# Performance work log

Hardware: AMD Instinct MI355X
Metric: run time of the kernel (lower is better)

## Reference

```python
import jax, jax.numpy as jnp
import numpy as np

N_OBJ = 256   # number of RoIs/objects
C = 151       # num_obj_classes (Visual Genome)
H = 512       # hidden_dim == output_dim
T = 3         # time_step


def setup_inputs() -> dict:
    key = jax.random.key(0)
    ks = jax.random.split(key, 12)
    s = jnp.float32(0.02)

    def lin(k, out_dim, in_dim):
        k1, k2 = jax.random.split(k)
        w = jax.random.normal(k1, (out_dim, in_dim), jnp.float32) * s
        b = jax.random.normal(k2, (out_dim,), jnp.float32) * s
        return w, b

    inp = {}
    inp['input_ggnn'] = jax.random.normal(ks[0], (N_OBJ, H), jnp.float32)
    inp['matrix'] = jax.random.uniform(ks[1], (C, C), jnp.float32)
    for i, name in enumerate(['eq3_w', 'eq3_u', 'eq4_w', 'eq4_u', 'eq5_w', 'eq5_u']):
        in_dim = 2 * H if name.endswith('_w') else H
        w, b = lin(ks[2 + i], H, in_dim)
        inp['w_' + name] = w
        inp['b_' + name] = b
    w, b = lin(ks[8], H, 2 * H)
    inp['w_out'], inp['b_out'] = w, b
    w, b = lin(ks[9], C, C * H)
    inp['w_cls'], inp['b_cls'] = w, b
    return inp


def _ggnn_obj(input_ggnn, matrix,
              w_eq3_w, b_eq3_w, w_eq3_u, b_eq3_u,
              w_eq4_w, b_eq4_w, w_eq4_u, b_eq4_u,
              w_eq5_w, b_eq5_w, w_eq5_u, b_eq5_u,
              w_out, b_out, w_cls, b_cls):
    n = input_ggnn.shape[0]
    # hidden[i, c] = input_ggnn[i] for every class slot c  -> [N, C, H]
    hidden0 = jnp.broadcast_to(input_ggnn[:, None, :], (n, C, H))

    def step(hidden, _):
        hidden_sum = hidden.sum(axis=0)                # [C, H]
        x = hidden_sum[None, :, :] - hidden            # [N, C, H]
        # matrix.T @ x_i  and  matrix @ x_i, vectorized over N
        av1 = jnp.einsum('cd,nch->ndh', matrix, x)     # M^T propagation
        av2 = jnp.einsum('dc,nch->ndh', matrix, x)     # M propagation
        av = jnp.concatenate([av1, av2], axis=-1).reshape(n * C, 2 * H)
        h = hidden.reshape(n * C, H)
        zv = jax.nn.sigmoid(av @ w_eq3_w.T + b_eq3_w + h @ w_eq3_u.T + b_eq3_u)
        rv = jax.nn.sigmoid(av @ w_eq4_w.T + b_eq4_w + h @ w_eq4_u.T + b_eq4_u)
        hv = jnp.tanh(av @ w_eq5_w.T + b_eq5_w + (rv * h) @ w_eq5_u.T + b_eq5_u)
        h = (1.0 - zv) * h + zv * hv
        return h.reshape(n, C, H), None

    hidden, _ = jax.lax.scan(step, hidden0, None, length=T)

    inp_rep = hidden0.reshape(n * C, H)                # input repeated per class slot
    out = jnp.concatenate([hidden.reshape(n * C, H), inp_rep], axis=1)  # [N*C, 2H]
    out = jax.nn.relu(out @ w_out.T + b_out)           # [N*C, H]
    obj_dists = out.reshape(n, C * H) @ w_cls.T + b_cls  # [N, C]
    return obj_dists


def reference(input_ggnn, matrix,
              w_eq3_w, b_eq3_w, w_eq3_u, b_eq3_u,
              w_eq4_w, b_eq4_w, w_eq4_u, b_eq4_u,
              w_eq5_w, b_eq5_w, w_eq5_u, b_eq5_u,
              w_out, b_out, w_cls, b_cls):
    return _ggnn_obj(input_ggnn, matrix,
                     w_eq3_w, b_eq3_w, w_eq3_u, b_eq3_u,
                     w_eq4_w, b_eq4_w, w_eq4_u, b_eq4_u,
                     w_eq5_w, b_eq5_w, w_eq5_u, b_eq5_u,
                     w_out, b_out, w_cls, b_cls)
```

## Files before the change

kernel.cpp:

```cpp
#include <hip/hip_runtime.h>


#define C_     151
#define H_     512
#define NOBJ   256
#define NR     38656
#define NCH    64
#define CH     9664
#define CHP    9728
#define KPAD   160
#define KLDS   168
#define KA     2560
#define KV     3584

typedef _Float16 half8 __attribute__((ext_vector_type(8)));
typedef _Float16 half4 __attribute__((ext_vector_type(4)));
typedef float    f32x4 __attribute__((ext_vector_type(4)));

__device__ __forceinline__ float sigm(float x) { return 1.f / (1.f + expf(-x)); }

__device__ __forceinline__ void gload16(const void* g, void* l) {
    __builtin_amdgcn_global_load_lds(
        (const __attribute__((address_space(1))) void*)g,
        (__attribute__((address_space(3))) void*)l, 16, 0, 0);
}

__device__ __forceinline__ half8 loadA8(const _Float16* p) { return *(const half8*)p; }
__device__ __forceinline__ half8 loadA8(const float* p) {
    f32x4 a = *(const f32x4*)p;
    f32x4 b = *(const f32x4*)(p + 4);
    half8 o;
    #pragma unroll
    for (int j = 0; j < 4; ++j) { o[j] = (_Float16)a[j]; o[4 + j] = (_Float16)b[j]; }
    return o;
}

template<int OP, typename AT, bool DUPK>
__global__ __launch_bounds__(256, 2)
void gemm_kernel(const AT* __restrict__ A, int lda,
                 const _Float16* __restrict__ B, int ldb,
                 void* __restrict__ Out, int ldo,
                 const float* __restrict__ bias,
                 const float* __restrict__ bias2,
                 int kchunk, int chunkStride)
{
    constexpr bool A16 = (sizeof(AT) == 2);
    __shared__ _Float16 sA[128 * 32];
    __shared__ _Float16 sB[128 * 32];
    const int tid  = threadIdx.x;
    const int lane = tid & 63;
    const int w    = tid >> 6;
    const int m0   = blockIdx.x * 128;
    const int n0   = blockIdx.y * 128;
    const int kbase = blockIdx.z * kchunk;

    const int s0 = tid, s1 = tid + 256;
    const AT* Ap0 = A + (size_t)(m0 + (s0 >> 2)) * lda + 8 * (s0 & 3);
    const AT* Ap1 = A + (size_t)(m0 + (s1 >> 2)) * lda + 8 * (s1 & 3);
    const _Float16* Bp0 = B + (size_t)(n0 + (s0 >> 2)) * ldb + kbase + 8 * (s0 & 3);
    const _Float16* Bp1 = B + (size_t)(n0 + (s1 >> 2)) * ldb + kbase + 8 * (s1 & 3);
    const int la0 = 8 * s0;
    const int la1 = 8 * s1;
    _Float16* lA0 = &sA[w * 512];
    _Float16* lA1 = &sA[2048 + w * 512];
    _Float16* lB0 = &sB[w * 512];
    _Float16* lB1 = &sB[2048 + w * 512];

    f32x4 acc[4][4];
    #pragma unroll
    for (int i = 0; i < 4; ++i)
        #pragma unroll
        for (int j = 0; j < 4; ++j)
            #pragma unroll
            for (int r = 0; r < 4; ++r) acc[i][j][r] = 0.f;

    const int mrow = (w >> 1) * 64;
    const int ncol = (w & 1) * 64;
    const int fra  = (lane & 15) * 32 + 8 * (lane >> 4);

    for (int k0 = 0; k0 < kchunk; k0 += 32) {
        int kA;
        if (DUPK) kA = (k0 < 2048) ? k0 : ((k0 < 3072) ? k0 - 2048 : k0 - 1024);
        else      kA = kbase + k0;
        if constexpr (A16) {
            __syncthreads();
            gload16(Ap0 + kA, lA0);
            gload16(Ap1 + kA, lA1);
            gload16(Bp0 + k0, lB0);
            gload16(Bp1 + k0, lB1);
            __syncthreads();
        } else {
            half8 va0 = loadA8(Ap0 + kA);
            half8 va1 = loadA8(Ap1 + kA);
            half8 vb0 = *(const half8*)(Bp0 + k0);
            half8 vb1 = *(const half8*)(Bp1 + k0);
            __syncthreads();
            *(half8*)&sA[la0] = va0;
            *(half8*)&sA[la1] = va1;
            *(half8*)&sB[la0] = vb0;
            *(half8*)&sB[la1] = vb1;
            __syncthreads();
        }
        half8 af[4], bf[4];
        #pragma unroll
        for (int i = 0; i < 4; ++i)
            af[i] = *(const half8*)&sA[(mrow + i * 16) * 32 + fra];
        #pragma unroll
        for (int i = 0; i < 4; ++i)
            bf[i] = *(const half8*)&sB[(ncol + i * 16) * 32 + fra];
        #pragma unroll
        for (int mi = 0; mi < 4; ++mi)
            #pragma unroll
            for (int ni = 0; ni < 4; ++ni)
                acc[mi][ni] = __builtin_amdgcn_mfma_f32_16x16x32_f16(af[mi], bf[ni], acc[mi][ni], 0, 0, 0);
    }

    const size_t zoff = (size_t)blockIdx.z * (size_t)chunkStride;
    #pragma unroll
    for (int mi = 0; mi < 4; ++mi) {
        #pragma unroll
        for (int ni = 0; ni < 4; ++ni) {
            #pragma unroll
            for (int r = 0; r < 4; ++r) {
                const int row = m0 + mrow + mi * 16 + (lane >> 4) * 4 + r;
                const int col = n0 + ncol + ni * 16 + (lane & 15);
                float v = acc[mi][ni][r];
                const size_t o = zoff + (size_t)row * ldo + col;
                if (OP == 0) {
                    ((float*)Out)[o] = v;
                } else if (OP == 1) {
                    ((_Float16*)Out)[o] = (_Float16)v;
                } else {
                    const unsigned n = (unsigned)row / 151u;
                    v += bias[col] + bias2[n * 512u + col];
                    v = v > 0.f ? v : 0.f;
                    ((_Float16*)Out)[o] = (_Float16)v;
                }
            }
        }
    }
}

template<int OP, bool DUPK>
__global__ __launch_bounds__(512, 2)
void gemm_wide(const _Float16* __restrict__ A, int lda,
               const _Float16* __restrict__ B, int ldb,
               void* __restrict__ Out, int ldo,
               int kchunk, int chunkStride)
{
    __shared__ _Float16 sA[128 * 32];
    __shared__ _Float16 sB[256 * 32];
    const int tid  = threadIdx.x;
    const int lane = tid & 63;
    const int w    = tid >> 6;
    const int m0   = blockIdx.x * 128;
    const int n0   = blockIdx.y * 256;
    const int kbase = blockIdx.z * kchunk;

    const _Float16* Ap = A + (size_t)(m0 + (tid >> 2)) * lda + 8 * (tid & 3);
    const _Float16* Bp0 = B + (size_t)(n0 + (tid >> 2)) * ldb + kbase + 8 * (tid & 3);
    const _Float16* Bp1 = B + (size_t)(n0 + 128 + (tid >> 2)) * ldb + kbase + 8 * (tid & 3);
    _Float16* lA  = &sA[w * 512];
    _Float16* lB0 = &sB[w * 512];
    _Float16* lB1 = &sB[4096 + w * 512];

    f32x4 acc[4][4];
    #pragma unroll
    for (int i = 0; i < 4; ++i)
        #pragma unroll
        for (int j = 0; j < 4; ++j)
            #pragma unroll
            for (int r = 0; r < 4; ++r) acc[i][j][r] = 0.f;

    const int mrow = (w >> 2) * 64;
    const int ncol = (w & 3) * 64;
    const int fra  = (lane & 15) * 32 + 8 * (lane >> 4);

    for (int k0 = 0; k0 < kchunk; k0 += 32) {
        int kA;
        if (DUPK) kA = (k0 < 2048) ? k0 : ((k0 < 3072) ? k0 - 2048 : k0 - 1024);
        else      kA = kbase + k0;
        __syncthreads();
        gload16(Ap + kA, lA);
        gload16(Bp0 + k0, lB0);
        gload16(Bp1 + k0, lB1);
        __syncthreads();
        half8 af[4], bf[4];
        #pragma unroll
        for (int i = 0; i < 4; ++i)
            af[i] = *(const half8*)&sA[(mrow + i * 16) * 32 + fra];
        #pragma unroll
        for (int i = 0; i < 4; ++i)
            bf[i] = *(const half8*)&sB[(ncol + i * 16) * 32 + fra];
        #pragma unroll
        for (int mi = 0; mi < 4; ++mi)
            #pragma unroll
            for (int ni = 0; ni < 4; ++ni)
                acc[mi][ni] = __builtin_amdgcn_mfma_f32_16x16x32_f16(af[mi], bf[ni], acc[mi][ni], 0, 0, 0);
    }

    const size_t zoff = (size_t)blockIdx.z * (size_t)chunkStride;
    #pragma unroll
    for (int mi = 0; mi < 4; ++mi) {
        #pragma unroll
        for (int ni = 0; ni < 4; ++ni) {
            #pragma unroll
            for (int r = 0; r < 4; ++r) {
                const int row = m0 + mrow + mi * 16 + (lane >> 4) * 4 + r;
                const int col = n0 + ncol + ni * 16 + (lane & 15);
                const float v = acc[mi][ni][r];
                const size_t o = zoff + (size_t)row * ldo + col;
                if (OP == 0) ((float*)Out)[o] = v;
                else         ((_Float16*)Out)[o] = (_Float16)v;
            }
        }
    }
}

__global__ __launch_bounds__(256, 2)
void mix_kernel(const _Float16* __restrict__ xh, const _Float16* __restrict__ xl,
                const _Float16* __restrict__ MTh, const _Float16* __restrict__ MTl,
                const _Float16* __restrict__ Mrh, const _Float16* __restrict__ Mrl,
                _Float16* __restrict__ AVH)
{
    __shared__ _Float16 sxh[64 * KLDS];
    __shared__ _Float16 sxl[64 * KLDS];
    const int n  = blockIdx.x;
    const int h0 = blockIdx.y * 64;
    const int tid = threadIdx.x;

    #pragma unroll
    for (int i = 0; i < 5; ++i) {
        const int s  = tid + 256 * i;
        const int c  = s >> 3;
        const int hg = s & 7;
        half8 vh = *(const half8*)&xh[(size_t)(n * C_ + c) * H_ + h0 + hg * 8];
        half8 vl = *(const half8*)&xl[(size_t)(n * C_ + c) * H_ + h0 + hg * 8];
        #pragma unroll
        for (int j = 0; j < 8; ++j) {
            sxh[(hg * 8 + j) * KLDS + c] = vh[j];
            sxl[(hg * 8 + j) * KLDS + c] = vl[j];
        }
    }
    __syncthreads();

    const int lane = tid & 63;
    const int w    = tid >> 6;
    const _Float16* Mhi = (w >> 1) ? Mrh : MTh;
    const _Float16* Mlo = (w >> 1) ? Mrl : MTl;
    const int hb = (w & 1) * 32;

    f32x4 acc[10][2];
    #pragma unroll
    for (int i = 0; i < 10; ++i)
        #pragma unroll
        for (int j = 0; j < 2; ++j)
            #pragma unroll
            for (int r = 0; r < 4; ++r) acc[i][j][r] = 0.f;

    #pragma unroll
    for (int pass = 0; pass < 3; ++pass) {
        const _Float16* Ma = (pass == 2) ? Mlo : Mhi;
        const _Float16* X  = (pass == 1) ? sxl : sxh;
        #pragma unroll
        for (int kk = 0; kk < 5; ++kk) {
            const int k0 = kk * 32;
            half8 bf[2];
            #pragma unroll
            for (int ht = 0; ht < 2; ++ht)
                bf[ht] = *(const half8*)&X[(hb + ht * 16 + (lane & 15)) * KLDS + k0 + 8 * (lane >> 4)];
            #pragma unroll
            for (int dt = 0; dt < 10; ++dt) {
                half8 af = *(const half8*)&Ma[(dt * 16 + (lane & 15)) * KPAD + k0 + 8 * (lane >> 4)];
                acc[dt][0] = __builtin_amdgcn_mfma_f32_16x16x32_f16(af, bf[0], acc[dt][0], 0, 0, 0);
                acc[dt][1] = __builtin_amdgcn_mfma_f32_16x16x32_f16(af, bf[1], acc[dt][1], 0, 0, 0);
            }
        }
    }

    const int mixoff = (w >> 1) * 512;
    #pragma unroll
    for (int dt = 0; dt < 10; ++dt) {
        #pragma unroll
        for (int ht = 0; ht < 2; ++ht) {
            #pragma unroll
            for (int r = 0; r < 4; ++r) {
                const int d = dt * 16 + (lane >> 4) * 4 + r;
                if (d < C_) {
                    const int h = h0 + hb + ht * 16 + (lane & 15);
                    const float v = acc[dt][ht][r];
                    const _Float16 hi = (_Float16)v;
                    const _Float16 lo = (_Float16)(v - (float)hi);
                    _Float16* rowp = AVH + (size_t)(n * C_ + d) * KA + mixoff + h;
                    rowp[0]    = hi;
                    rowp[1024] = lo;
                }
            }
        }
    }
}


__global__ void k_sreduce(const float* __restrict__ hid, float* __restrict__ Stmp)
{
    const int c  = blockIdx.x;
    const int g  = blockIdx.y;
    const int hw = threadIdx.x;
    const float* p = hid + (size_t)c * H_ + hw * 8;
    float s[8];
    #pragma unroll
    for (int j = 0; j < 8; ++j) s[j] = 0.f;
    const size_t stride = (size_t)C_ * H_;
    for (int n = g * 32; n < g * 32 + 32; ++n) {
        f32x4 a = *(const f32x4*)(p + (size_t)n * stride);
        f32x4 b = *(const f32x4*)(p + (size_t)n * stride + 4);
        #pragma unroll
        for (int j = 0; j < 4; ++j) { s[j] += a[j]; s[4 + j] += b[j]; }
    }
    float* o = Stmp + (size_t)g * (C_ * H_) + c * H_ + hw * 8;
    *(f32x4*)o       = f32x4{s[0], s[1], s[2], s[3]};
    *(f32x4*)(o + 4) = f32x4{s[4], s[5], s[6], s[7]};
}

__global__ void k_sfold(const float* __restrict__ Stmp, float* __restrict__ S)
{
    const int idx = blockIdx.x * 256 + threadIdx.x;
    float s = 0.f;
    #pragma unroll
    for (int g = 0; g < 8; ++g) s += Stmp[(size_t)g * (C_ * H_) + idx];
    S[idx] = s;
}

__global__ void k_xcast(const float* __restrict__ hid, const float* __restrict__ S,
                        _Float16* __restrict__ xh, _Float16* __restrict__ xl,
                        _Float16* __restrict__ AVH, int cbase)
{
    const int idx = blockIdx.x * 256 + threadIdx.x;
    const unsigned r = idx >> 6;
    const int h = (idx & 63) * 8;
    half8 oh, ol, hh;
    if (r < CH) {
        const unsigned c = r % 151u;
        const float* hp = &hid[(size_t)(cbase + r) * H_ + h];
        const float* sp = &S[c * H_ + h];
        #pragma unroll
        for (int j = 0; j < 8; ++j) {
            const float hv = hp[j];
            const float x = sp[j] - hv;
            const _Float16 hi = (_Float16)x;
            oh[j] = hi;
            ol[j] = (_Float16)(x - (float)hi);
            hh[j] = (_Float16)hv;
        }
    } else {
        #pragma unroll
        for (int j = 0; j < 8; ++j) { oh[j] = (_Float16)0.f; ol[j] = (_Float16)0.f; hh[j] = (_Float16)0.f; }
    }
    *(half8*)&xh[(size_t)r * H_ + h] = oh;
    *(half8*)&xl[(size_t)r * H_ + h] = ol;
    *(half8*)&AVH[(size_t)r * KA + 2048 + h] = hh;
}

__global__ void k_ew1(_Float16* __restrict__ pre, const float* __restrict__ hid,
                      const float* __restrict__ bz, const float* __restrict__ br, int cbase)
{
    const int idx = blockIdx.x * 256 + threadIdx.x;
    const unsigned r = idx >> 7;
    const int o4 = (idx & 127) << 2;
    const size_t base = (size_t)r * 1536;
    half4 zp = *(const half4*)&pre[base + o4];
    half4 rp = *(const half4*)&pre[base + 512 + o4];
    f32x4 hd = *(const f32x4*)&hid[(size_t)(cbase + r) * H_ + o4];
    f32x4 bz4 = *(const f32x4*)&bz[o4];
    f32x4 br4 = *(const f32x4*)&br[o4];
    half4 zs, rh;
    #pragma unroll
    for (int j = 0; j < 4; ++j) {
        float z = sigm((float)zp[j] + bz4[j]);
        float rr = sigm((float)rp[j] + br4[j]);
        zs[j] = (_Float16)z;
        rh[j] = (_Float16)(rr * hd[j]);
    }
    *(half4*)&pre[base + o4] = zs;
    *(half4*)&pre[base + 512 + o4] = rh;
}

__global__ void k_ew2(const _Float16* __restrict__ pre, const _Float16* __restrict__ p5u,
                      float* __restrict__ hid, const float* __restrict__ b5, int cbase)
{
    const int idx = blockIdx.x * 256 + threadIdx.x;
    const unsigned r = idx >> 7;
    const int o4 = (idx & 127) << 2;
    const size_t base = (size_t)r * 1536;
    half4 w5 = *(const half4*)&pre[base + 1024 + o4];
    half4 p5 = *(const half4*)&p5u[(size_t)r * H_ + o4];
    half4 zz = *(const half4*)&pre[base + o4];
    f32x4 hd = *(const f32x4*)&hid[(size_t)(cbase + r) * H_ + o4];
    f32x4 b54 = *(const f32x4*)&b5[o4];
    #pragma unroll
    for (int j = 0; j < 4; ++j) {
        float t = tanhf((float)w5[j] + (float)p5[j] + b54[j]);
        float z = (float)zz[j];
        hd[j] = (1.f - z) * hd[j] + z * t;
    }
    *(f32x4*)&hid[(size_t)(cbase + r) * H_ + o4] = hd;
}


__global__ void prep_wbig(const float* w3w, const float* w3u,
                          const float* w4w, const float* w4u,
                          const float* w5w, const float* w5u,
                          _Float16* __restrict__ Wbig)
{
    const int idx = blockIdx.x * 256 + threadIdx.x;
    const int op = idx / KV;
    const int j = idx - op * KV;
    const int g = op >> 9, o = op & 511;
    const float* ww = (g == 0) ? w3w : (g == 1) ? w4w : w5w;
    const float* wu = (g == 0) ? w3u : (g == 1) ? w4u : w5u;
    _Float16 out;
    if (j < 1024) {
        out = (_Float16)ww[o * 1024 + j];
    } else if (j < 2048) {
        out = (_Float16)ww[o * 1024 + (j - 1024)];
    } else if (j < 3072) {
        const float v = ww[o * 1024 + (j - 2048)];
        const _Float16 hi = (_Float16)v;
        out = (_Float16)(v - (float)hi);
    } else {
        out = (g < 2) ? (_Float16)wu[o * 512 + (j - 3072)] : (_Float16)0.f;
    }
    Wbig[idx] = out;
}

__global__ void prep_m(const float* __restrict__ matrix,
                       _Float16* __restrict__ MTh, _Float16* __restrict__ MTl,
                       _Float16* __restrict__ Mrh, _Float16* __restrict__ Mrl)
{
    const int idx = blockIdx.x * 256 + threadIdx.x;
    const int d = idx / KPAD, c = idx - d * KPAD;
    float vT = 0.f, vR = 0.f;
    if (d < C_ && c < C_) { vT = matrix[c * C_ + d]; vR = matrix[d * C_ + c]; }
    const _Float16 th = (_Float16)vT;
    const _Float16 rh = (_Float16)vR;
    MTh[idx] = th; MTl[idx] = (_Float16)(vT - (float)th);
    Mrh[idx] = rh; Mrl[idx] = (_Float16)(vR - (float)rh);
}

__global__ void prep_wout(const float* __restrict__ wout,
                          _Float16* __restrict__ WL, _Float16* __restrict__ WR)
{
    const int idx = blockIdx.x * 256 + threadIdx.x;
    const int o = idx >> 9, j = idx & 511;
    WL[idx] = (_Float16)wout[o * 1024 + j];
    WR[idx] = (_Float16)wout[o * 1024 + 512 + j];
}

__global__ void prep_wcls(const float* __restrict__ wcls, _Float16* __restrict__ w16)
{
    const int k = blockIdx.x * 256 + threadIdx.x;
    const int d = blockIdx.y;
    _Float16 v = (_Float16)0.f;
    if (d < C_) v = (_Float16)wcls[(size_t)d * (C_ * H_) + k];
    w16[(size_t)d * (C_ * H_) + k] = v;
}

__global__ void k_cast(const float* __restrict__ src, _Float16* __restrict__ dst, int n)
{
    const int i = blockIdx.x * 256 + threadIdx.x;
    if (i < n) dst[i] = (_Float16)src[i];
}

__global__ void prep_bias(const float* b3w, const float* b3u, const float* b4w,
                          const float* b4u, const float* b5w, const float* b5u,
                          float* bz, float* br, float* b5)
{
    const int i = threadIdx.x;
    bz[i] = b3w[i] + b3u[i];
    br[i] = b4w[i] + b4u[i];
    b5[i] = b5w[i] + b5u[i];
}

__global__ void prep_hid(const float* __restrict__ input, float* __restrict__ hid)
{
    const int idx = blockIdx.x * 256 + threadIdx.x;
    const unsigned row = idx >> 7;
    const int h4 = (idx & 127) << 2;
    const unsigned n = row / 151u;
    f32x4 v = *(const f32x4*)&input[(size_t)n * H_ + h4];
    *(f32x4*)&hid[(size_t)row * H_ + h4] = v;
}

__global__ void k_reduce(const float* __restrict__ partial, const float* __restrict__ bcls,
                         float* __restrict__ out)
{
    const int idx = blockIdx.x * 256 + threadIdx.x;
    const unsigned n = (unsigned)idx / 151u;
    const unsigned d = (unsigned)idx - n * 151u;
    float s = 0.f;
    for (int z = 0; z < C_; ++z)
        s += partial[(size_t)z * (NOBJ * 256) + n * 256 + d];
    out[idx] = s + bcls[d];
}


extern "C" void kernel_launch(void* const* d_in, const int* in_sizes, int n_in,
                              void* d_out, int out_size, void* d_ws, size_t ws_size,
                              hipStream_t stream)
{
    const float* input  = (const float*)d_in[0];
    const float* matrix = (const float*)d_in[1];
    const float* w3w = (const float*)d_in[2];
    const float* b3w = (const float*)d_in[3];
    const float* w3u = (const float*)d_in[4];
    const float* b3u = (const float*)d_in[5];
    const float* w4w = (const float*)d_in[6];
    const float* b4w = (const float*)d_in[7];
    const float* w4u = (const float*)d_in[8];
    const float* b4u = (const float*)d_in[9];
    const float* w5w = (const float*)d_in[10];
    const float* b5w = (const float*)d_in[11];
    const float* w5u = (const float*)d_in[12];
    const float* b5u = (const float*)d_in[13];
    const float* wout = (const float*)d_in[14];
    const float* bout = (const float*)d_in[15];
    const float* wcls = (const float*)d_in[16];
    const float* bcls = (const float*)d_in[17];
    float* obj = (float*)d_out;

    char* ws = (char*)d_ws;
    size_t off = 0;
    auto take = [&](size_t bytes) -> char* {
        off = (off + 255) & ~(size_t)255;
        char* p = ws + off;
        off += bytes;
        return p;
    };

    _Float16* Wbig  = (_Float16*)take((size_t)1536 * KV * 2);
    _Float16* MTh   = (_Float16*)take((size_t)KPAD * KPAD * 2);
    _Float16* MTl   = (_Float16*)take((size_t)KPAD * KPAD * 2);
    _Float16* Mrh   = (_Float16*)take((size_t)KPAD * KPAD * 2);
    _Float16* Mrl   = (_Float16*)take((size_t)KPAD * KPAD * 2);
    _Float16* W5u16 = (_Float16*)take((size_t)512 * 512 * 2);
    _Float16* WL16  = (_Float16*)take((size_t)512 * 512 * 2);
    _Float16* WR16  = (_Float16*)take((size_t)512 * 512 * 2);
    _Float16* in16  = (_Float16*)take((size_t)256 * 512 * 2);
    float*    bz    = (float*)take(512 * 4);
    float*    br    = (float*)take(512 * 4);
    float*    b5    = (float*)take(512 * 4);
    float*    Stmp  = (float*)take((size_t)8 * C_ * H_ * 4);
    float*    S32   = (float*)take((size_t)C_ * H_ * 4);
    float*    base  = (float*)take((size_t)256 * 512 * 4);
    float*    hid32 = (float*)take((size_t)NR * H_ * 4);
    _Float16* AVH   = (_Float16*)take((size_t)CHP * KA * 2);
    _Float16* prec  = (_Float16*)take((size_t)CHP * 1536 * 2);
    _Float16* xh = prec;
    _Float16* xl = prec + (size_t)CHP * H_;
    _Float16* p5u = AVH;
    _Float16* OUT16 = AVH;
    _Float16* Wcls16 = (_Float16*)hid32;
    float* partial = (float*)((char*)hid32 + (size_t)NOBJ * C_ * H_ * 2);

    (void)in_sizes; (void)n_in; (void)out_size; (void)ws_size;

    prep_wbig<<<dim3((1536 * KV) / 256), 256, 0, stream>>>(w3w, w3u, w4w, w4u, w5w, w5u, Wbig);
    prep_m<<<dim3((KPAD * KPAD) / 256), 256, 0, stream>>>(matrix, MTh, MTl, Mrh, Mrl);
    k_cast<<<dim3((512 * 512) / 256), 256, 0, stream>>>(w5u, W5u16, 512 * 512);
    prep_wout<<<dim3((512 * 512) / 256), 256, 0, stream>>>(wout, WL16, WR16);
    k_cast<<<dim3((256 * 512) / 256), 256, 0, stream>>>(input, in16, 256 * 512);
    prep_bias<<<dim3(1), 512, 0, stream>>>(b3w, b3u, b4w, b4u, b5w, b5u, bz, br, b5);
    prep_hid<<<dim3((NR * 128) / 256), 256, 0, stream>>>(input, hid32);
    gemm_kernel<0, _Float16, false><<<dim3(2, 4, 1), 256, 0, stream>>>(
        in16, 512, WR16, 512, base, 512, nullptr, nullptr, 512, 0);

    for (int t = 0; t < 3; ++t) {
        k_sreduce<<<dim3(C_, 8), 64, 0, stream>>>(hid32, Stmp);
        k_sfold<<<dim3((C_ * H_) / 256), 256, 0, stream>>>(Stmp, S32);
        for (int cc = 0; cc < 4; ++cc) {
            const int cbase = cc * CH;
            k_xcast<<<dim3((CHP * 64) / 256), 256, 0, stream>>>(hid32, S32, xh, xl, AVH, cbase);
            mix_kernel<<<dim3(NCH, 8), 256, 0, stream>>>(xh, xl, MTh, MTl, Mrh, Mrl, AVH);
            gemm_wide<1, true><<<dim3(CHP / 128, 1536 / 256, 1), 512, 0, stream>>>(
                AVH, KA, Wbig, KV, prec, 1536, KV, 0);
            k_ew1<<<dim3((CH * 128) / 256), 256, 0, stream>>>(prec, hid32, bz, br, cbase);
            gemm_wide<1, false><<<dim3(CHP / 128, 512 / 256, 1), 512, 0, stream>>>(
                prec + 512, 1536, W5u16, 512, p5u, 512, 512, 0);
            k_ew2<<<dim3((CH * 128) / 256), 256, 0, stream>>>(prec, p5u, hid32, b5, cbase);
        }
    }

    gemm_kernel<2, float, false><<<dim3(NR / 128, 512 / 128, 1), 256, 0, stream>>>(
        hid32, 512, WL16, 512, OUT16, 512, bout, base, 512, 0);

    prep_wcls<<<dim3((C_ * H_) / 256, 256), 256, 0, stream>>>(wcls, Wcls16);
    gemm_kernel<0, _Float16, false><<<dim3(NOBJ / 128, 256 / 128, C_), 256, 0, stream>>>(
        OUT16, C_ * H_, Wcls16, C_ * H_, partial, 256, nullptr, nullptr, 512, NOBJ * 256);
    k_reduce<<<dim3(NR / 256), 256, 0, stream>>>(partial, bcls, obj);
}
```

Baseline: 2.971 ms.

## Swizzle GEMM LDS layout, fuse xcast into mix kernel, split-K the W5u GEMM

Applies an XOR-style swizzle to the K-quarter placement of global-to-LDS loads and fragment reads in both GEMM kernels, aiming to reduce LDS bank conflicts. Folds the k_xcast conversion (S minus hidden, hi/lo fp16 split, hidden cast into AVH) directly into mix_kernel, which removes one launch and the xh/xl round trip through global memory. Replaces the wide W5u GEMM with a 2-way split-K gemm_kernel launch that writes two partial outputs, and k_ew2 now sums both. Split-K adds an extra partial-buffer read, and mix_kernel now does more scattered fp32 loads.

Measured after the change: 2.777 ms. 1.07x faster.

```diff
diff --git a/kernel.cpp b/kernel.cpp
--- a/kernel.cpp
+++ b/kernel.cpp
@@ -25,6 +25,14 @@
         (__attribute__((address_space(3))) void*)l, 16, 0, 0);
 }
 
+__device__ __forceinline__ int kqswz(int s) {
+    return 8 * (((s & 3) + 8 - ((s >> 2) & 3) - ((s >> 4) & 3)) & 3);
+}
+__device__ __forceinline__ int fraswz(int lane) {
+    const int lb = lane & 15;
+    return lb * 32 + 8 * (((lane >> 4) + lb + (lb >> 2)) & 3);
+}
+
 __device__ __forceinline__ half8 loadA8(const _Float16* p) { return *(const half8*)p; }
 __device__ __forceinline__ half8 loadA8(const float* p) {
     f32x4 a = *(const f32x4*)p;
@@ -55,10 +63,10 @@
     const int kbase = blockIdx.z * kchunk;
 
     const int s0 = tid, s1 = tid + 256;
-    const AT* Ap0 = A + (size_t)(m0 + (s0 >> 2)) * lda + 8 * (s0 & 3);
-    const AT* Ap1 = A + (size_t)(m0 + (s1 >> 2)) * lda + 8 * (s1 & 3);
-    const _Float16* Bp0 = B + (size_t)(n0 + (s0 >> 2)) * ldb + kbase + 8 * (s0 & 3);
-    const _Float16* Bp1 = B + (size_t)(n0 + (s1 >> 2)) * ldb + kbase + 8 * (s1 & 3);
+    const AT* Ap0 = A + (size_t)(m0 + (s0 >> 2)) * lda + kqswz(s0);
+    const AT* Ap1 = A + (size_t)(m0 + (s1 >> 2)) * lda + kqswz(s1);
+    const _Float16* Bp0 = B + (size_t)(n0 + (s0 >> 2)) * ldb + kbase + kqswz(s0);
+    const _Float16* Bp1 = B + (size_t)(n0 + (s1 >> 2)) * ldb + kbase + kqswz(s1);
     const int la0 = 8 * s0;
     const int la1 = 8 * s1;
     _Float16* lA0 = &sA[w * 512];
@@ -76,7 +84,7 @@
 
     const int mrow = (w >> 1) * 64;
     const int ncol = (w & 1) * 64;
-    const int fra  = (lane & 15) * 32 + 8 * (lane >> 4);
+    const int fra  = fraswz(lane);
 
     for (int k0 = 0; k0 < kchunk; k0 += 32) {
         int kA;
@@ -157,9 +165,10 @@
     const int n0   = blockIdx.y * 256;
     const int kbase = blockIdx.z * kchunk;
 
-    const _Float16* Ap = A + (size_t)(m0 + (tid >> 2)) * lda + 8 * (tid & 3);
-    const _Float16* Bp0 = B + (size_t)(n0 + (tid >> 2)) * ldb + kbase + 8 * (tid & 3);
-    const _Float16* Bp1 = B + (size_t)(n0 + 128 + (tid >> 2)) * ldb + kbase + 8 * (tid & 3);
+    const int kq = kqswz(tid);
+    const _Float16* Ap = A + (size_t)(m0 + (tid >> 2)) * lda + kq;
+    const _Float16* Bp0 = B + (size_t)(n0 + (tid >> 2)) * ldb + kbase + kq;
+    const _Float16* Bp1 = B + (size_t)(n0 + 128 + (tid >> 2)) * ldb + kbase + kq;
     _Float16* lA  = &sA[w * 512];
     _Float16* lB0 = &sB[w * 512];
     _Float16* lB1 = &sB[4096 + w * 512];
@@ -174,7 +183,7 @@
 
     const int mrow = (w >> 2) * 64;
     const int ncol = (w & 3) * 64;
-    const int fra  = (lane & 15) * 32 + 8 * (lane >> 4);
+    const int fra  = fraswz(lane);
 
     for (int k0 = 0; k0 < kchunk; k0 += 32) {
         int kA;
@@ -218,10 +227,10 @@
 }
 
 __global__ __launch_bounds__(256, 2)
-void mix_kernel(const _Float16* __restrict__ xh, const _Float16* __restrict__ xl,
+void mix_kernel(const float* __restrict__ hid, const float* __restrict__ S,
                 const _Float16* __restrict__ MTh, const _Float16* __restrict__ MTl,
                 const _Float16* __restrict__ Mrh, const _Float16* __restrict__ Mrl,
-                _Float16* __restrict__ AVH)
+                _Float16* __restrict__ AVH, int cbase)
 {
     __shared__ _Float16 sxh[64 * KLDS];
     __shared__ _Float16 sxl[64 * KLDS];
@@ -234,12 +243,29 @@
         const int s  = tid + 256 * i;
         const int c  = s >> 3;
         const int hg = s & 7;
-        half8 vh = *(const half8*)&xh[(size_t)(n * C_ + c) * H_ + h0 + hg * 8];
-        half8 vl = *(const half8*)&xl[(size_t)(n * C_ + c) * H_ + h0 + hg * 8];
+        half8 oh, ol;
+        if (c < C_) {
+            const float* hp = &hid[(size_t)(cbase + n * C_ + c) * H_ + h0 + hg * 8];
+            const float* sp = &S[c * H_ + h0 + hg * 8];
+            half8 hh;
+            #pragma unroll
+            for (int j = 0; j < 8; ++j) {
+                const float hv = hp[j];
+                const float x = sp[j] - hv;
+                const _Float16 hi = (_Float16)x;
+                oh[j] = hi;
+                ol[j] = (_Float16)(x - (float)hi);
+                hh[j] = (_Float16)hv;
+            }
+            *(half8*)&AVH[(size_t)(n * C_ + c) * KA + 2048 + h0 + hg * 8] = hh;
+        } else {
+            #pragma unroll
+            for (int j = 0; j < 8; ++j) { oh[j] = (_Float16)0.f; ol[j] = (_Float16)0.f; }
+        }
         #pragma unroll
         for (int j = 0; j < 8; ++j) {
-            sxh[(hg * 8 + j) * KLDS + c] = vh[j];
-            sxl[(hg * 8 + j) * KLDS + c] = vl[j];
+            sxh[(hg * 8 + j) * KLDS + c] = oh[j];
+            sxl[(hg * 8 + j) * KLDS + c] = ol[j];
         }
     }
     __syncthreads();
@@ -331,36 +357,6 @@
     S[idx] = s;
 }
 
-__global__ void k_xcast(const float* __restrict__ hid, const float* __restrict__ S,
-                        _Float16* __restrict__ xh, _Float16* __restrict__ xl,
-                        _Float16* __restrict__ AVH, int cbase)
-{
-    const int idx = blockIdx.x * 256 + threadIdx.x;
-    const unsigned r = idx >> 6;
-    const int h = (idx & 63) * 8;
-    half8 oh, ol, hh;
-    if (r < CH) {
-        const unsigned c = r % 151u;
-        const float* hp = &hid[(size_t)(cbase + r) * H_ + h];
-        const float* sp = &S[c * H_ + h];
-        #pragma unroll
-        for (int j = 0; j < 8; ++j) {
-            const float hv = hp[j];
-            const float x = sp[j] - hv;
-            const _Float16 hi = (_Float16)x;
-            oh[j] = hi;
-            ol[j] = (_Float16)(x - (float)hi);
-            hh[j] = (_Float16)hv;
-        }
-    } else {
-        #pragma unroll
-        for (int j = 0; j < 8; ++j) { oh[j] = (_Float16)0.f; ol[j] = (_Float16)0.f; hh[j] = (_Float16)0.f; }
-    }
-    *(half8*)&xh[(size_t)r * H_ + h] = oh;
-    *(half8*)&xl[(size_t)r * H_ + h] = ol;
-    *(half8*)&AVH[(size_t)r * KA + 2048 + h] = hh;
-}
-
 __global__ void k_ew1(_Float16* __restrict__ pre, const float* __restrict__ hid,
                       const float* __restrict__ bz, const float* __restrict__ br, int cbase)
 {
@@ -385,7 +381,8 @@
     *(half4*)&pre[base + 512 + o4] = rh;
 }
 
-__global__ void k_ew2(const _Float16* __restrict__ pre, const _Float16* __restrict__ p5u,
+__global__ void k_ew2(const _Float16* __restrict__ pre, const _Float16* __restrict__ p5a,
+                      const _Float16* __restrict__ p5b,
                       float* __restrict__ hid, const float* __restrict__ b5, int cbase)
 {
     const int idx = blockIdx.x * 256 + threadIdx.x;
@@ -393,13 +390,14 @@
     const int o4 = (idx & 127) << 2;
     const size_t base = (size_t)r * 1536;
     half4 w5 = *(const half4*)&pre[base + 1024 + o4];
-    half4 p5 = *(const half4*)&p5u[(size_t)r * H_ + o4];
+    half4 pa = *(const half4*)&p5a[(size_t)r * H_ + o4];
+    half4 pb = *(const half4*)&p5b[(size_t)r * H_ + o4];
     half4 zz = *(const half4*)&pre[base + o4];
     f32x4 hd = *(const f32x4*)&hid[(size_t)(cbase + r) * H_ + o4];
     f32x4 b54 = *(const f32x4*)&b5[o4];
     #pragma unroll
     for (int j = 0; j < 4; ++j) {
-        float t = tanhf((float)w5[j] + (float)p5[j] + b54[j]);
+        float t = tanhf((float)w5[j] + (float)pa[j] + (float)pb[j] + b54[j]);
         float z = (float)zz[j];
         hd[j] = (1.f - z) * hd[j] + z * t;
     }
@@ -555,8 +553,6 @@
     float*    hid32 = (float*)take((size_t)NR * H_ * 4);
     _Float16* AVH   = (_Float16*)take((size_t)CHP * KA * 2);
     _Float16* prec  = (_Float16*)take((size_t)CHP * 1536 * 2);
-    _Float16* xh = prec;
-    _Float16* xl = prec + (size_t)CHP * H_;
     _Float16* p5u = AVH;
     _Float16* OUT16 = AVH;
     _Float16* Wcls16 = (_Float16*)hid32;
@@ -579,14 +575,15 @@
         k_sfold<<<dim3((C_ * H_) / 256), 256, 0, stream>>>(Stmp, S32);
         for (int cc = 0; cc < 4; ++cc) {
             const int cbase = cc * CH;
-            k_xcast<<<dim3((CHP * 64) / 256), 256, 0, stream>>>(hid32, S32, xh, xl, AVH, cbase);
-            mix_kernel<<<dim3(NCH, 8), 256, 0, stream>>>(xh, xl, MTh, MTl, Mrh, Mrl, AVH);
+            mix_kernel<<<dim3(NCH, 8), 256, 0, stream>>>(
+                hid32, S32, MTh, MTl, Mrh, Mrl, AVH, cbase);
             gemm_wide<1, true><<<dim3(CHP / 128, 1536 / 256, 1), 512, 0, stream>>>(
                 AVH, KA, Wbig, KV, prec, 1536, KV, 0);
             k_ew1<<<dim3((CH * 128) / 256), 256, 0, stream>>>(prec, hid32, bz, br, cbase);
-            gemm_wide<1, false><<<dim3(CHP / 128, 512 / 256, 1), 512, 0, stream>>>(
-                prec + 512, 1536, W5u16, 512, p5u, 512, 512, 0);
-            k_ew2<<<dim3((CH * 128) / 256), 256, 0, stream>>>(prec, p5u, hid32, b5, cbase);
+            gemm_kernel<1, _Float16, false><<<dim3(CHP / 128, 4, 2), 256, 0, stream>>>(
+                prec + 512, 1536, W5u16, 512, p5u, 512, nullptr, nullptr, 256, CHP * 512);
+            k_ew2<<<dim3((CH * 128) / 256), 256, 0, stream>>>(
+                prec, p5u, p5u + (size_t)CHP * 512, hid32, b5, cbase);
         }
     }
 
```
